# Kernel optimization log

Hardware: AMD Instinct MI355X
Metric: run time of the kernel (lower is better)

The kernel has to match this reference:

```python
import jax, jax.numpy as jnp
import numpy as np

D_MODEL = 768
MIMO_RANK = 4


def setup_inputs() -> dict:
    key = jax.random.key(0)
    ks = jax.random.split(key, 6)
    B, T, D, R = 2, 2048, D_MODEL, MIMO_RANK
    x = jax.random.normal(ks[0], (B, T, D), dtype=jnp.float32)
    norm_w = jnp.ones((D,), dtype=jnp.float32)
    W_in = jax.random.normal(ks[1], (D * R * 2, D), dtype=jnp.float32) * 0.02
    W_out = jax.random.normal(ks[2], (D, D), dtype=jnp.float32) * 0.02
    a_param = jax.random.normal(ks[3], (D, R, 2), dtype=jnp.float32) * 0.12
    b_param = jax.random.normal(ks[4], (D, R, 2), dtype=jnp.float32) * 0.15
    c_param = jax.random.normal(ks[5], (D, R, 2), dtype=jnp.float32) * 0.15
    return {"x": x, "norm_w": norm_w, "W_in": W_in, "W_out": W_out,
            "a_param": a_param, "b_param": b_param, "c_param": c_param}


def reference(x, norm_w, W_in, W_out, a_param, b_param, c_param):
    B, T, D = x.shape
    R = a_param.shape[1]
    # RMSNorm
    xn = x * jax.lax.rsqrt(jnp.mean(x * x, axis=-1, keepdims=True) + 1e-6) * norm_w
    # in_proj -> interleaved complex MIMO input u: [B,T,D,R,2]
    u = (xn @ W_in.T).reshape(B, T, D, R, 2)
    # coefficients (tanh-bounded; |a| scaled by 0.97 for stability)
    a = jnp.tanh(a_param) * 0.97
    b = jnp.tanh(b_param)
    c = jnp.tanh(c_param)
    ac = jax.lax.complex(a[..., 0], a[..., 1])  # [D,R]
    bc = jax.lax.complex(b[..., 0], b[..., 1])
    cc = jax.lax.complex(c[..., 0], c[..., 1])
    uc = jax.lax.complex(u[..., 0], u[..., 1])  # [B,T,D,R]
    # linear complex recurrence s_t = a * s_{t-1} + b * u_t, zero init state,
    # parallelized with an associative scan over time.
    bu = bc[None, None] * uc
    A = jnp.broadcast_to(ac[None, None], bu.shape)

    def comb(l, r):
        return (l[0] * r[0], r[0] * l[1] + r[1])

    _, s = jax.lax.associative_scan(comb, (A, bu), axis=1)  # [B,T,D,R] complex
    # output mix: real part of c * h, summed over MIMO rank -> [B,T,D]
    y = jnp.real(cc[None, None] * s).sum(axis=-1)
    return y @ W_out.T
```

## Files before the change

### kernel.cpp

```cpp
#include <hip/hip_runtime.h>
#include <hip/hip_bf16.h>
#include <stdint.h>

#define BATCH 2
#define TT 2048
#define DM 768
#define RR 4
#define M_TOK 4096
#define NFEAT 6144
#define NCH 6144
#define CHUNK 64
#define NCHUNK 32

typedef __attribute__((ext_vector_type(8))) short short8;
typedef __attribute__((ext_vector_type(4))) float float4v;

__device__ inline float bf2f(uint32_t bits16) {
    union { uint32_t u; float f; } x; x.u = bits16 << 16; return x.f;
}

typedef const __attribute__((address_space(1))) void* gptr_t;
typedef __attribute__((address_space(3))) void* lptr_t;

__device__ inline void async_ld16(const void* g, void* l) {
    __builtin_amdgcn_global_load_lds((gptr_t)(uintptr_t)g, (lptr_t)(uintptr_t)l,
                                     16, 0, 0);
}

__device__ inline uint2 pack4bf(float a, float b, float c, float d) {
    union { __hip_bfloat16 h[4]; uint2 u; } o;
    o.h[0] = __float2bfloat16(a); o.h[1] = __float2bfloat16(b);
    o.h[2] = __float2bfloat16(c); o.h[3] = __float2bfloat16(d);
    return o.u;
}

__device__ inline void cstep(float& sr, float& si, float2 a, float2 bb,
                             uint32_t uw) {
    float ur = bf2f(uw & 0xffffu), ui = bf2f(uw >> 16);
    float tr = bb.x * ur - bb.y * ui;
    float ti = bb.x * ui + bb.y * ur;
    float nr = a.x * sr - a.y * si + tr;
    float ni = a.x * si + a.y * sr + ti;
    sr = nr; si = ni;
}

__global__ __launch_bounds__(256) void prep_rms(
    const float* __restrict__ x, const float* __restrict__ w,
    const float* __restrict__ W_in, const float* __restrict__ W_out,
    const float* __restrict__ ap, const float* __restrict__ bp,
    const float* __restrict__ cp,
    __hip_bfloat16* __restrict__ xn,
    __hip_bfloat16* __restrict__ Win_bf, __hip_bfloat16* __restrict__ Wout_bf,
    float2* __restrict__ ac, float2* __restrict__ bc,
    float2* __restrict__ cc, float2* __restrict__ aL) {
    int bid = blockIdx.x;
    int tid = threadIdx.x;
    if (bid < M_TOK) {
        __shared__ float wsum[3];
        float4 v = make_float4(0.f, 0.f, 0.f, 0.f);
        if (tid < 192) v = ((const float4*)(x + (size_t)bid * DM))[tid];
        float ss = v.x * v.x + v.y * v.y + v.z * v.z + v.w * v.w;
        #pragma unroll
        for (int o = 1; o < 64; o <<= 1) ss += __shfl_xor(ss, o);
        if (tid < 192 && (tid & 63) == 0) wsum[tid >> 6] = ss;
        __syncthreads();
        if (tid < 192) {
            float tot = wsum[0] + wsum[1] + wsum[2];
            float scale = rsqrtf(tot * (1.f / DM) + 1e-6f);
            float4 wv = ((const float4*)w)[tid];
            ((uint2*)(xn + (size_t)bid * DM))[tid] =
                pack4bf(v.x * scale * wv.x, v.y * scale * wv.y,
                        v.z * scale * wv.z, v.w * scale * wv.w);
        }
        return;
    }
    const int N1 = NFEAT * DM / 4;
    const int N2 = DM * DM / 4;
    int i = (bid - M_TOK) * 256 + tid;
    if (i < N1) {
        float4 v = ((const float4*)W_in)[i];
        ((uint2*)Win_bf)[i] = pack4bf(v.x, v.y, v.z, v.w);
    } else if (i < N1 + N2) {
        int k = i - N1;
        float4 v = ((const float4*)W_out)[k];
        ((uint2*)Wout_bf)[k] = pack4bf(v.x, v.y, v.z, v.w);
    }
    if (i < DM * RR) {
        float ar = tanhf(ap[2 * i])     * 0.97f;
        float ai = tanhf(ap[2 * i + 1]) * 0.97f;
        ac[i] = make_float2(ar, ai);
        bc[i] = make_float2(tanhf(bp[2 * i]), tanhf(bp[2 * i + 1]));
        cc[i] = make_float2(tanhf(cp[2 * i]), tanhf(cp[2 * i + 1]));
        float xr = ar, xi = ai;
        #pragma unroll
        for (int k = 0; k < 6; ++k) {
            float nr = xr * xr - xi * xi;
            float ni = 2.f * xr * xi;
            xr = nr; xi = ni;
        }
        aL[i] = make_float2(xr, xi);
    }
}

__global__ __launch_bounds__(256) void gemm_in_scan(
    const __hip_bfloat16* __restrict__ A, const __hip_bfloat16* __restrict__ B,
    __hip_bfloat16* __restrict__ C,
    const float2* __restrict__ ac, const float2* __restrict__ bc,
    float2* __restrict__ chunkEnd) {
    constexpr int BM = 128, BN = 128, BK = 64;
    constexpr int MI = BM / 32, NJ = BN / 32, CPR = BK / 8;
    constexpr int K = DM;
    __shared__ __attribute__((aligned(16))) __hip_bfloat16 smem[BM * BK + BN * BK];
    __hip_bfloat16* lA = smem;
    __hip_bfloat16* lB = smem + BM * BK;
    const int tid  = threadIdx.x;
    const int lane = tid & 63;
    const int wave = tid >> 6;
    const int quad = lane >> 4;
    const int l15  = lane & 15;
    const int wm = (wave >> 1) * (BM / 2);
    const int wn = (wave & 1) * (BN / 2);
    const int m0 = blockIdx.y * BM;
    const int n0 = blockIdx.x * BN;

    float4v acc[MI][NJ] = {};

    for (int k0 = 0; k0 < K; k0 += BK) {
        __syncthreads();
        #pragma unroll
        for (int it = 0; it < BM * CPR / 256; ++it) {
            int p = it * 256 + tid;
            int row = p / CPR;
            int cg = (p & (CPR - 1)) ^ (row & (CPR - 1));
            async_ld16(A + (size_t)(m0 + row) * K + k0 + cg * 8, lA + p * 8);
        }
        #pragma unroll
        for (int it = 0; it < BN * CPR / 256; ++it) {
            int p = it * 256 + tid;
            int row = p / CPR;
            int cg = (p & (CPR - 1)) ^ (row & (CPR - 1));
            async_ld16(B + (size_t)(n0 + row) * K + k0 + cg * 8, lB + p * 8);
        }
        __syncthreads();
        #pragma unroll
        for (int s = 0; s < BK / 32; ++s) {
            short8 af[MI], bfr[NJ];
            #pragma unroll
            for (int i = 0; i < MI; ++i) {
                int r = wm + i * 16 + l15;
                int c = (s * 4 + quad) ^ (r & (CPR - 1));
                af[i] = *(const short8*)(lA + r * BK + c * 8);
            }
            #pragma unroll
            for (int j = 0; j < NJ; ++j) {
                int r = wn + j * 16 + l15;
                int c = (s * 4 + quad) ^ (r & (CPR - 1));
                bfr[j] = *(const short8*)(lB + r * BK + c * 8);
            }
            #pragma unroll
            for (int i = 0; i < MI; ++i)
                #pragma unroll
                for (int j = 0; j < NJ; ++j)
                    acc[i][j] = __builtin_amdgcn_mfma_f32_16x16x32_bf16(
                        af[i], bfr[j], acc[i][j], 0, 0, 0);
        }
    }
    __syncthreads();
    #pragma unroll
    for (int i = 0; i < MI; ++i)
        #pragma unroll
        for (int j = 0; j < NJ; ++j)
            #pragma unroll
            for (int rg = 0; rg < 4; ++rg) {
                int row = wm + i * 16 + quad * 4 + rg;
                int col = wn + j * 16 + l15;
                float v = acc[i][j][rg];
                __hip_bfloat16 h = __float2bfloat16(v);
                C[(size_t)(m0 + row) * NFEAT + n0 + col] = h;
                int pc = (((col >> 3) ^ (row & 15)) << 3) | (col & 7);
                smem[row * BN + pc] = h;
            }
    __syncthreads();
    if (tid < 128) {
        int ch    = tid & 63;
        int chunk = tid >> 6;
        int rem = n0 / 2 + ch;
        int b = m0 >= TT;
        int jg = ((m0 & (TT - 1)) >> 6) + chunk;
        float2 a = ac[rem], bb = bc[rem];
        float sr = 0.f, si = 0.f;
        int col = 2 * ch;
        int cchunk = col >> 3, cin = col & 7;
        int t0 = chunk * 64;
        #pragma unroll 8
        for (int t = 0; t < 64; ++t) {
            int row = t0 + t;
            int pc = ((cchunk ^ (row & 15)) << 3) | cin;
            uint32_t val = *(const uint32_t*)(smem + row * BN + pc);
            cstep(sr, si, a, bb, val);
        }
        chunkEnd[(size_t)jg * NCH + b * (DM * RR) + rem] = make_float2(sr, si);
    }
}

__global__ __launch_bounds__(256) void gemm_out(
    const __hip_bfloat16* __restrict__ A, const __hip_bfloat16* __restrict__ B,
    float* __restrict__ C) {
    constexpr int BM = 64, BN = 64, BK = 128;
    constexpr int MI = BM / 32, NJ = BN / 32, CPR = BK / 8;
    constexpr int K = DM;
    __shared__ __attribute__((aligned(16))) __hip_bfloat16 lA[BM * BK];
    __shared__ __attribute__((aligned(16))) __hip_bfloat16 lB[BN * BK];
    const int tid  = threadIdx.x;
    const int lane = tid & 63;
    const int wave = tid >> 6;
    const int quad = lane >> 4;
    const int l15  = lane & 15;
    const int wm = (wave >> 1) * (BM / 2);
    const int wn = (wave & 1) * (BN / 2);
    const int m0 = blockIdx.y * BM;
    const int n0 = blockIdx.x * BN;

    float4v acc[MI][NJ] = {};

    for (int k0 = 0; k0 < K; k0 += BK) {
        __syncthreads();
        #pragma unroll
        for (int it = 0; it < BM * CPR / 256; ++it) {
            int p = it * 256 + tid;
            int row = p / CPR;
            int cg = (p & (CPR - 1)) ^ (row & (CPR - 1));
            async_ld16(A + (size_t)(m0 + row) * K + k0 + cg * 8, lA + p * 8);
        }
        #pragma unroll
        for (int it = 0; it < BN * CPR / 256; ++it) {
            int p = it * 256 + tid;
            int row = p / CPR;
            int cg = (p & (CPR - 1)) ^ (row & (CPR - 1));
            async_ld16(B + (size_t)(n0 + row) * K + k0 + cg * 8, lB + p * 8);
        }
        __syncthreads();
        #pragma unroll
        for (int s = 0; s < BK / 32; ++s) {
            short8 af[MI], bfr[NJ];
            #pragma unroll
            for (int i = 0; i < MI; ++i) {
                int r = wm + i * 16 + l15;
                int c = (s * 4 + quad) ^ (r & (CPR - 1));
                af[i] = *(const short8*)(lA + r * BK + c * 8);
            }
            #pragma unroll
            for (int j = 0; j < NJ; ++j) {
                int r = wn + j * 16 + l15;
                int c = (s * 4 + quad) ^ (r & (CPR - 1));
                bfr[j] = *(const short8*)(lB + r * BK + c * 8);
            }
            #pragma unroll
            for (int i = 0; i < MI; ++i)
                #pragma unroll
                for (int j = 0; j < NJ; ++j)
                    acc[i][j] = __builtin_amdgcn_mfma_f32_16x16x32_bf16(
                        af[i], bfr[j], acc[i][j], 0, 0, 0);
        }
    }
    #pragma unroll
    for (int i = 0; i < MI; ++i)
        #pragma unroll
        for (int j = 0; j < NJ; ++j)
            #pragma unroll
            for (int rg = 0; rg < 4; ++rg) {
                int row = m0 + wm + i * 16 + quad * 4 + rg;
                int col = n0 + wn + j * 16 + l15;
                C[(size_t)row * DM + col] = acc[i][j][rg];
            }
}

__global__ __launch_bounds__(256) void scan_passC(
    const uint4* __restrict__ u4,
    const float2* __restrict__ ac, const float2* __restrict__ bc,
    const float2* __restrict__ cc, const float2* __restrict__ aLp,
    const float2* __restrict__ chunkEnd,
    __hip_bfloat16* __restrict__ y) {
    int g = blockIdx.x * 256 + threadIdx.x;
    int j = blockIdx.y;
    int b = g >= DM;
    int d = g - b * DM;
    int cb = d * RR;
    float2 a0 = ac[cb], a1 = ac[cb + 1], a2 = ac[cb + 2], a3 = ac[cb + 3];
    float2 b0 = bc[cb], b1 = bc[cb + 1], b2 = bc[cb + 2], b3 = bc[cb + 3];
    float2 c0 = cc[cb], c1 = cc[cb + 1], c2 = cc[cb + 2], c3 = cc[cb + 3];
    float2 aL0 = aLp[cb], aL1 = aLp[cb + 1], aL2 = aLp[cb + 2], aL3 = aLp[cb + 3];
    float s0r = 0, s0i = 0, s1r = 0, s1i = 0;
    float s2r = 0, s2i = 0, s3r = 0, s3i = 0;
    for (int jj = 0; jj < j; ++jj) {
        size_t eb = (size_t)jj * NCH + b * (DM * RR) + cb;
        float2 e0 = chunkEnd[eb],     e1 = chunkEnd[eb + 1];
        float2 e2 = chunkEnd[eb + 2], e3 = chunkEnd[eb + 3];
        float nr, ni;
        nr = aL0.x * s0r - aL0.y * s0i + e0.x; ni = aL0.x * s0i + aL0.y * s0r + e0.y; s0r = nr; s0i = ni;
        nr = aL1.x * s1r - aL1.y * s1i + e1.x; ni = aL1.x * s1i + aL1.y * s1r + e1.y; s1r = nr; s1i = ni;
        nr = aL2.x * s2r - aL2.y * s2i + e2.x; ni = aL2.x * s2i + aL2.y * s2r + e2.y; s2r = nr; s2i = ni;
        nr = aL3.x * s3r - aL3.y * s3i + e3.x; ni = aL3.x * s3i + aL3.y * s3r + e3.y; s3r = nr; s3i = ni;
    }
    size_t base = ((size_t)(b * TT + j * CHUNK)) * DM + d;
    #pragma unroll 4
    for (int i = 0; i < CHUNK; ++i) {
        uint4 uw = u4[base + (size_t)i * DM];
        cstep(s0r, s0i, a0, b0, uw.x);
        cstep(s1r, s1i, a1, b1, uw.y);
        cstep(s2r, s2i, a2, b2, uw.z);
        cstep(s3r, s3i, a3, b3, uw.w);
        float yv = c0.x * s0r - c0.y * s0i + c1.x * s1r - c1.y * s1i
                 + c2.x * s2r - c2.y * s2i + c3.x * s3r - c3.y * s3i;
        y[base + (size_t)i * DM] = __float2bfloat16(yv);
    }
}

extern "C" void kernel_launch(void* const* d_in, const int* in_sizes, int n_in,
                              void* d_out, int out_size, void* d_ws,
                              size_t ws_size, hipStream_t stream) {
    const float* x      = (const float*)d_in[0];
    const float* norm_w = (const float*)d_in[1];
    const float* W_in   = (const float*)d_in[2];
    const float* W_out  = (const float*)d_in[3];
    const float* a_p    = (const float*)d_in[4];
    const float* b_p    = (const float*)d_in[5];
    const float* c_p    = (const float*)d_in[6];
    float* out = (float*)d_out;

    char* ws = (char*)d_ws;
    size_t off = 0;
    auto alloc = [&](size_t bytes) {
        void* p = ws + off;
        off += (bytes + 255) & ~(size_t)255;
        return p;
    };
    __hip_bfloat16* Win_bf  = (__hip_bfloat16*)alloc((size_t)NFEAT * DM * 2);
    __hip_bfloat16* Wout_bf = (__hip_bfloat16*)alloc((size_t)DM * DM * 2);
    __hip_bfloat16* xn      = (__hip_bfloat16*)alloc((size_t)M_TOK * DM * 2);
    __hip_bfloat16* u       = (__hip_bfloat16*)alloc((size_t)M_TOK * NFEAT * 2);
    __hip_bfloat16* y       = (__hip_bfloat16*)alloc((size_t)M_TOK * DM * 2);
    float2* ac = (float2*)alloc((size_t)DM * RR * 8);
    float2* bc = (float2*)alloc((size_t)DM * RR * 8);
    float2* cc = (float2*)alloc((size_t)DM * RR * 8);
    float2* aL = (float2*)alloc((size_t)DM * RR * 8);
    float2* chunkEnd = (float2*)alloc((size_t)NCHUNK * NCH * 8);

    {
        int cast_blocks = ((NFEAT * DM + DM * DM) / 4 + 255) / 256;
        prep_rms<<<M_TOK + cast_blocks, 256, 0, stream>>>(
            x, norm_w, W_in, W_out, a_p, b_p, c_p,
            xn, Win_bf, Wout_bf, ac, bc, cc, aL);
    }
    gemm_in_scan<<<dim3(NFEAT / 128, M_TOK / 128), 256, 0, stream>>>(
        xn, Win_bf, u, ac, bc, chunkEnd);
    scan_passC<<<dim3(BATCH * DM / 256, NCHUNK), 256, 0, stream>>>(
        (const uint4*)u, ac, bc, cc, aL, chunkEnd, y);
    gemm_out<<<dim3(DM / 64, M_TOK / 64), 256, 0, stream>>>(
        y, Wout_bf, out);
}
```

Measured before the change: 195.6 us.

## Compute local chunk outputs in GEMM epilogue and drop u materialization

The in-projection GEMM epilogue now runs the within-chunk scan, mixes each state with c, reduces over rank with lane shuffles, and writes a small per-chunk local output y_local in fp32 instead of the full bf16 u tensor. The second pass no longer rereads u. It adds the carried-in state's contribution as c*a^(t+1)*carry, advancing that term by one complex multiply per step. This removes writing and reading the large u buffer (M_TOK x 6144 bf16). The cost is extra shuffles and LDS writes inside the GEMM epilogue, plus an fp32 y_local buffer.

```diff
diff --git a/kernel.cpp b/kernel.cpp
--- a/kernel.cpp
+++ b/kernel.cpp
@@ -32,6 +32,10 @@
     o.h[0] = __float2bfloat16(a); o.h[1] = __float2bfloat16(b);
     o.h[2] = __float2bfloat16(c); o.h[3] = __float2bfloat16(d);
     return o.u;
+}
+
+__device__ inline float2 cmul(float2 a, float2 b) {
+    return make_float2(a.x * b.x - a.y * b.y, a.x * b.y + a.y * b.x);
 }
 
 __device__ inline void cstep(float& sr, float& si, float2 a, float2 bb,
@@ -104,13 +108,15 @@
 
 __global__ __launch_bounds__(256) void gemm_in_scan(
     const __hip_bfloat16* __restrict__ A, const __hip_bfloat16* __restrict__ B,
-    __hip_bfloat16* __restrict__ C,
     const float2* __restrict__ ac, const float2* __restrict__ bc,
+    const float2* __restrict__ cc,
+    float* __restrict__ y_local,
     float2* __restrict__ chunkEnd) {
     constexpr int BM = 128, BN = 128, BK = 64;
     constexpr int MI = BM / 32, NJ = BN / 32, CPR = BK / 8;
     constexpr int K = DM;
     __shared__ __attribute__((aligned(16))) __hip_bfloat16 smem[BM * BK + BN * BK];
+    __shared__ __attribute__((aligned(16))) float y_loc[BM * 16];
     __hip_bfloat16* lA = smem;
     __hip_bfloat16* lB = smem + BM * BK;
     const int tid  = threadIdx.x;
@@ -174,9 +180,7 @@
             for (int rg = 0; rg < 4; ++rg) {
                 int row = wm + i * 16 + quad * 4 + rg;
                 int col = wn + j * 16 + l15;
-                float v = acc[i][j][rg];
-                __hip_bfloat16 h = __float2bfloat16(v);
-                C[(size_t)(m0 + row) * NFEAT + n0 + col] = h;
+                __hip_bfloat16 h = __float2bfloat16(acc[i][j][rg]);
                 int pc = (((col >> 3) ^ (row & 15)) << 3) | (col & 7);
                 smem[row * BN + pc] = h;
             }
@@ -187,19 +191,34 @@
         int rem = n0 / 2 + ch;
         int b = m0 >= TT;
         int jg = ((m0 & (TT - 1)) >> 6) + chunk;
-        float2 a = ac[rem], bb = bc[rem];
+        float2 a = ac[rem], bb = bc[rem], cf = cc[rem];
         float sr = 0.f, si = 0.f;
         int col = 2 * ch;
         int cchunk = col >> 3, cin = col & 7;
         int t0 = chunk * 64;
+        int dloc = ch >> 2;
+        bool isr0 = (ch & 3) == 0;
         #pragma unroll 8
         for (int t = 0; t < 64; ++t) {
             int row = t0 + t;
             int pc = ((cchunk ^ (row & 15)) << 3) | cin;
             uint32_t val = *(const uint32_t*)(smem + row * BN + pc);
             cstep(sr, si, a, bb, val);
+            float v = cf.x * sr - cf.y * si;
+            v += __shfl_xor(v, 1);
+            v += __shfl_xor(v, 2);
+            if (isr0) y_loc[row * 16 + dloc] = v;
         }
         chunkEnd[(size_t)jg * NCH + b * (DM * RR) + rem] = make_float2(sr, si);
+    }
+    __syncthreads();
+    {
+        int t = tid >> 1;
+        int half = tid & 1;
+        const float4* src = (const float4*)(y_loc + t * 16 + half * 8);
+        float4* dst = (float4*)(y_local + (size_t)(m0 + t) * DM + n0 / 8 + half * 8);
+        dst[0] = src[0];
+        dst[1] = src[1];
     }
 }
 
@@ -276,10 +295,9 @@
 }
 
 __global__ __launch_bounds__(256) void scan_passC(
-    const uint4* __restrict__ u4,
-    const float2* __restrict__ ac, const float2* __restrict__ bc,
-    const float2* __restrict__ cc, const float2* __restrict__ aLp,
-    const float2* __restrict__ chunkEnd,
+    const float* __restrict__ y_local,
+    const float2* __restrict__ ac, const float2* __restrict__ cc,
+    const float2* __restrict__ aLp, const float2* __restrict__ chunkEnd,
     __hip_bfloat16* __restrict__ y) {
     int g = blockIdx.x * 256 + threadIdx.x;
     int j = blockIdx.y;
@@ -287,32 +305,29 @@
     int d = g - b * DM;
     int cb = d * RR;
     float2 a0 = ac[cb], a1 = ac[cb + 1], a2 = ac[cb + 2], a3 = ac[cb + 3];
-    float2 b0 = bc[cb], b1 = bc[cb + 1], b2 = bc[cb + 2], b3 = bc[cb + 3];
-    float2 c0 = cc[cb], c1 = cc[cb + 1], c2 = cc[cb + 2], c3 = cc[cb + 3];
     float2 aL0 = aLp[cb], aL1 = aLp[cb + 1], aL2 = aLp[cb + 2], aL3 = aLp[cb + 3];
-    float s0r = 0, s0i = 0, s1r = 0, s1i = 0;
-    float s2r = 0, s2i = 0, s3r = 0, s3i = 0;
+    float2 k0 = make_float2(0, 0), k1 = k0, k2 = k0, k3 = k0;
     for (int jj = 0; jj < j; ++jj) {
         size_t eb = (size_t)jj * NCH + b * (DM * RR) + cb;
         float2 e0 = chunkEnd[eb],     e1 = chunkEnd[eb + 1];
         float2 e2 = chunkEnd[eb + 2], e3 = chunkEnd[eb + 3];
         float nr, ni;
-        nr = aL0.x * s0r - aL0.y * s0i + e0.x; ni = aL0.x * s0i + aL0.y * s0r + e0.y; s0r = nr; s0i = ni;
-        nr = aL1.x * s1r - aL1.y * s1i + e1.x; ni = aL1.x * s1i + aL1.y * s1r + e1.y; s1r = nr; s1i = ni;
-        nr = aL2.x * s2r - aL2.y * s2i + e2.x; ni = aL2.x * s2i + aL2.y * s2r + e2.y; s2r = nr; s2i = ni;
-        nr = aL3.x * s3r - aL3.y * s3i + e3.x; ni = aL3.x * s3i + aL3.y * s3r + e3.y; s3r = nr; s3i = ni;
-    }
+        nr = aL0.x * k0.x - aL0.y * k0.y + e0.x; ni = aL0.x * k0.y + aL0.y * k0.x + e0.y; k0 = make_float2(nr, ni);
+        nr = aL1.x * k1.x - aL1.y * k1.y + e1.x; ni = aL1.x * k1.y + aL1.y * k1.x + e1.y; k1 = make_float2(nr, ni);
+        nr = aL2.x * k2.x - aL2.y * k2.y + e2.x; ni = aL2.x * k2.y + aL2.y * k2.x + e2.y; k2 = make_float2(nr, ni);
+        nr = aL3.x * k3.x - aL3.y * k3.y + e3.x; ni = aL3.x * k3.y + aL3.y * k3.x + e3.y; k3 = make_float2(nr, ni);
+    }
+    float2 q0 = cmul(cmul(cc[cb],     k0), a0);
+    float2 q1 = cmul(cmul(cc[cb + 1], k1), a1);
+    float2 q2 = cmul(cmul(cc[cb + 2], k2), a2);
+    float2 q3 = cmul(cmul(cc[cb + 3], k3), a3);
     size_t base = ((size_t)(b * TT + j * CHUNK)) * DM + d;
     #pragma unroll 4
     for (int i = 0; i < CHUNK; ++i) {
-        uint4 uw = u4[base + (size_t)i * DM];
-        cstep(s0r, s0i, a0, b0, uw.x);
-        cstep(s1r, s1i, a1, b1, uw.y);
-        cstep(s2r, s2i, a2, b2, uw.z);
-        cstep(s3r, s3i, a3, b3, uw.w);
-        float yv = c0.x * s0r - c0.y * s0i + c1.x * s1r - c1.y * s1i
-                 + c2.x * s2r - c2.y * s2i + c3.x * s3r - c3.y * s3i;
+        float yv = y_local[base + (size_t)i * DM] + q0.x + q1.x + q2.x + q3.x;
         y[base + (size_t)i * DM] = __float2bfloat16(yv);
+        q0 = cmul(q0, a0); q1 = cmul(q1, a1);
+        q2 = cmul(q2, a2); q3 = cmul(q3, a3);
     }
 }
 
@@ -338,7 +353,7 @@
     __hip_bfloat16* Win_bf  = (__hip_bfloat16*)alloc((size_t)NFEAT * DM * 2);
     __hip_bfloat16* Wout_bf = (__hip_bfloat16*)alloc((size_t)DM * DM * 2);
     __hip_bfloat16* xn      = (__hip_bfloat16*)alloc((size_t)M_TOK * DM * 2);
-    __hip_bfloat16* u       = (__hip_bfloat16*)alloc((size_t)M_TOK * NFEAT * 2);
+    float*          y_local = (float*)alloc((size_t)M_TOK * DM * 4);
     __hip_bfloat16* y       = (__hip_bfloat16*)alloc((size_t)M_TOK * DM * 2);
     float2* ac = (float2*)alloc((size_t)DM * RR * 8);
     float2* bc = (float2*)alloc((size_t)DM * RR * 8);
@@ -353,9 +368,9 @@
             xn, Win_bf, Wout_bf, ac, bc, cc, aL);
     }
     gemm_in_scan<<<dim3(NFEAT / 128, M_TOK / 128), 256, 0, stream>>>(
-        xn, Win_bf, u, ac, bc, chunkEnd);
+        xn, Win_bf, ac, bc, cc, y_local, chunkEnd);
     scan_passC<<<dim3(BATCH * DM / 256, NCHUNK), 256, 0, stream>>>(
-        (const uint4*)u, ac, bc, cc, aL, chunkEnd, y);
+        y_local, ac, cc, aL, chunkEnd, y);
     gemm_out<<<dim3(DM / 64, M_TOK / 64), 256, 0, stream>>>(
         y, Wout_bf, out);
 }
```

Measured after the change: 193.7 us. No clear change (-1.0%).
